# Performance work log

Hardware: AMD Instinct MI355X
Metric: run time of the kernel (lower is better)

The kernel has to match this reference:

```python
import jax, jax.numpy as jnp
import numpy as np

P_TOKENS = 200  # num_prompt_tokens
N_HEADS = 4


def setup_inputs() -> dict:
    key = jax.random.key(0)
    ks = jax.random.split(key, 6)
    B, N, C = 64, 1224, 1024
    D = 256  # bottleneck / down_size
    s = 0.02
    return {
        "x": jax.random.normal(ks[0], (B, N, C), dtype=jnp.float32),
        "down_W": jax.random.normal(ks[1], (D, C), dtype=jnp.float32) * s,
        "down_b": jnp.zeros((D,), jnp.float32),
        "up_W": jax.random.normal(ks[2], (C, D), dtype=jnp.float32) * s,
        "up_b": jnp.zeros((C,), jnp.float32),
        "in_proj_W": jax.random.normal(ks[3], (3 * D, D), dtype=jnp.float32) * s,
        "in_proj_b": jnp.zeros((3 * D,), jnp.float32),
        "out_proj_W": jax.random.normal(ks[4], (D, D), dtype=jnp.float32) * s,
        "out_proj_b": jnp.zeros((D,), jnp.float32),
        "gate": jnp.float32(1.0),
    }


def _forward(x, down_W, down_b, up_W, up_b, in_proj_W, in_proj_b,
             out_proj_W, out_proj_b, gate):
    B, N, C = x.shape
    E = down_W.shape[0]
    hd = E // N_HEADS
    # down projection + exact GELU (torch nn.GELU default)
    down = jax.nn.gelu(x @ down_W.T + down_b, approximate=False)  # [B,N,E]
    prompt = down[:, :P_TOKENS, :]   # [B,P,E]
    tok = down[:, P_TOKENS:, :]      # [B,T,E]
    # --- nn.MultiheadAttention(prompt, prompt, prompt) ---
    qkv = prompt @ in_proj_W.T + in_proj_b            # [B,P,3E]
    q, k, v = jnp.split(qkv, 3, axis=-1)
    def heads(t):
        return t.reshape(B, P_TOKENS, N_HEADS, hd)
    q, k, v = heads(q), heads(k), heads(v)
    attn = jnp.einsum('bqhd,bkhd->bhqk', q, k) / jnp.sqrt(jnp.float32(hd))
    attn = jax.nn.softmax(attn, axis=-1)
    sa = jnp.einsum('bhqk,bkhd->bqhd', attn, v).reshape(B, P_TOKENS, E)
    sa = sa @ out_proj_W.T + out_proj_b               # [B,P,E]
    # --- manual cross attention prompt -> tokens ---
    scale = jnp.float32(E) ** -0.5
    cross = jax.nn.softmax(jnp.einsum('bpe,bte->bpt', sa, tok) * scale, axis=-1)
    prompt_out = jnp.einsum('bpt,bte->bpe', cross, tok)  # [B,P,E]
    combined = jnp.concatenate([prompt_out, tok], axis=1)  # [B,N,E]
    up = combined @ up_W.T + up_b                          # [B,N,C]
    return gate * up


def reference(x, down_W, down_b, up_W, up_b, in_proj_W, in_proj_b,
              out_proj_W, out_proj_b, gate):
    return _forward(x, down_W, down_b, up_W, up_b, in_proj_W, in_proj_b,
                    out_proj_W, out_proj_b, gate)
```

## Files before the change

### kernel.cpp

```cpp
#include <hip/hip_runtime.h>
#include <math.h>

#define BB 64
#define NN 1224
#define CC 1024
#define DD 256
#define PP 200
#define TT 1024
#define HH 4
#define HDD 64

typedef __attribute__((ext_vector_type(8))) short bf16x8;
typedef __attribute__((ext_vector_type(4))) float f32x4;
typedef unsigned short u16;
typedef unsigned long long u64;

__device__ __forceinline__ u16 f2bf(float f) {
  union { float f; unsigned int u; } v; v.f = f;
  unsigned int r = v.u + 0x7FFF + ((v.u >> 16) & 1);
  return (u16)(r >> 16);
}
__device__ __forceinline__ float bf2f(u16 h) {
  union { unsigned int u; float f; } v; v.u = ((unsigned int)h) << 16;
  return v.f;
}
__device__ __forceinline__ unsigned int pk2(float a, float b) {
  return (unsigned int)f2bf(a) | ((unsigned int)f2bf(b) << 16);
}
__device__ __forceinline__ void gload16(const void* g, void* l) {
  __builtin_amdgcn_global_load_lds(
      (const __attribute__((address_space(1))) void*)g,
      (__attribute__((address_space(3))) void*)l, 16, 0, 0);
}

static const size_t SZ_DOWN = (size_t)BB * NN * DD * 2;
static const size_t SZ_TOKT = (size_t)BB * DD * TT * 2;
static const size_t SZ_Q    = (size_t)BB * HH * PP * HDD * 2;
static const size_t SZ_SCORES = (size_t)BB * PP * TT * 2;

static const size_t B_DOWN   = 0;
static const size_t B_TOKT   = B_DOWN + SZ_DOWN;
static const size_t B_POOL   = B_TOKT + SZ_TOKT;
static const size_t B_QB     = B_POOL;
static const size_t B_KB     = B_QB + SZ_Q;
static const size_t B_VB     = B_KB + SZ_Q;
static const size_t B_SA     = B_VB + SZ_Q;
static const size_t B_SA2    = B_SA + SZ_Q;
static const size_t B_PBF    = B_POOL;
static const size_t B_POUTBF = B_SA2;
static const size_t B_SCORES = B_SA2 + SZ_Q;
static const size_t B_W      = B_SCORES + SZ_SCORES * 2;
static const size_t B_WD     = B_W;
static const size_t B_WU     = B_WD + 524288;
static const size_t B_WIP    = B_WU + 524288;
static const size_t B_WOP    = B_WIP + 393216;

#define GEMM_VARS \
  const int tid = threadIdx.x; \
  const int lane = tid & 63, wave = tid >> 6; \
  const int wm = wave >> 2, wn = wave & 3; \
  f32x4 acc[4][4] = {};

#define MFMA_STEP(Ab, Bb) \
  _Pragma("unroll") \
  for (int kk = 0; kk < 64; kk += 32) { \
    bf16x8 af[4], bfr[4]; \
    _Pragma("unroll") \
    for (int mi = 0; mi < 4; ++mi) { \
      const int R = wm * 64 + mi * 16 + (lane & 15); \
      const int byt = (R * 128 + (kk + (lane >> 4) * 8) * 2) ^ ((R & 7) << 4); \
      af[mi] = *(const bf16x8*)((const char*)Ab + byt); \
    } \
    _Pragma("unroll") \
    for (int ni = 0; ni < 4; ++ni) { \
      const int R = wn * 64 + ni * 16 + (lane & 15); \
      const int byt = (R * 128 + (kk + (lane >> 4) * 8) * 2) ^ ((R & 7) << 4); \
      bfr[ni] = *(const bf16x8*)((const char*)Bb + byt); \
    } \
    _Pragma("unroll") \
    for (int mi = 0; mi < 4; ++mi) \
      _Pragma("unroll") \
      for (int ni = 0; ni < 4; ++ni) \
        acc[mi][ni] = __builtin_amdgcn_mfma_f32_16x16x32_bf16(af[mi], bfr[ni], acc[mi][ni], 0, 0, 0); \
  }

#define GLOAD_A2(Ab, SRC) \
  _Pragma("unroll") \
  for (int ii = 0; ii < 2; ++ii) { \
    const int slot = wave * 2 + ii; \
    const int L = slot * 1024 + lane * 16; \
    const int r = L >> 7; \
    const int ce = ((L & 127) ^ ((r & 7) << 4)) >> 1; \
    gload16((SRC), (char*)Ab + slot * 1024); \
  }

#define GLOAD_B4(Bb, SRC) \
  _Pragma("unroll") \
  for (int ii = 0; ii < 4; ++ii) { \
    const int slot = wave * 4 + ii; \
    const int L = slot * 1024 + lane * 16; \
    const int r = L >> 7; \
    const int ce = ((L & 127) ^ ((r & 7) << 4)) >> 1; \
    gload16((SRC), (char*)Bb + slot * 1024); \
  }

#define MFMA_STEP64(Ab, Bb) \
  _Pragma("unroll") \
  for (int kk = 0; kk < 64; kk += 32) { \
    bf16x8 af[4], bfr[2]; \
    _Pragma("unroll") \
    for (int mi = 0; mi < 4; ++mi) { \
      const int R = mi * 16 + (lane & 15); \
      const int byt = (R * 128 + (kk + (lane >> 4) * 8) * 2) ^ ((R & 7) << 4); \
      af[mi] = *(const bf16x8*)((const char*)Ab + byt); \
    } \
    _Pragma("unroll") \
    for (int ni = 0; ni < 2; ++ni) { \
      const int R = wave * 32 + ni * 16 + (lane & 15); \
      const int byt = (R * 128 + (kk + (lane >> 4) * 8) * 2) ^ ((R & 7) << 4); \
      bfr[ni] = *(const bf16x8*)((const char*)Bb + byt); \
    } \
    _Pragma("unroll") \
    for (int mi = 0; mi < 4; ++mi) \
      _Pragma("unroll") \
      for (int ni = 0; ni < 2; ++ni) \
        acc[mi][ni] = __builtin_amdgcn_mfma_f32_16x16x32_bf16(af[mi], bfr[ni], acc[mi][ni], 0, 0, 0); \
  }

#define GLOAD_A1(Ab, SRC) \
  { \
    const int L = wave * 1024 + lane * 16; \
    const int r = L >> 7; \
    const int ce = ((L & 127) ^ ((r & 7) << 4)) >> 1; \
    gload16((SRC), (char*)Ab + wave * 1024); \
  }

__global__ __launch_bounds__(256) void k_castw(const float* __restrict__ dW,
                                               const float* __restrict__ uW,
                                               const float* __restrict__ iW,
                                               const float* __restrict__ oW,
                                               u16* __restrict__ dWb, u16* __restrict__ uWb,
                                               u16* __restrict__ iWb, u16* __restrict__ oWb)
{
  const int id = blockIdx.x * 256 + threadIdx.x;
  const float* s; u16* d; int off;
  if (id < 65536)       { s = dW; d = dWb; off = id; }
  else if (id < 131072) { s = uW; d = uWb; off = id - 65536; }
  else if (id < 180224) { s = iW; d = iWb; off = id - 131072; }
  else                  { s = oW; d = oWb; off = id - 180224; }
  const float4 v = ((const float4*)s)[off];
  uint2 p; p.x = pk2(v.x, v.y); p.y = pk2(v.z, v.w);
  *(uint2*)&d[(size_t)off * 4] = p;
}

__global__ __launch_bounds__(512, 6) void k_down(const float* __restrict__ x,
                                                 const u16* __restrict__ Wd,
                                                 const float* __restrict__ bias,
                                                 u16* __restrict__ out)
{
  __shared__ u16 Ab[64 * 64];
  __shared__ u16 Bb[256 * 64];
  const int tid = threadIdx.x;
  const int lane = tid & 63, wave = tid >> 6;
  f32x4 acc[4][2] = {};
  const int m0 = blockIdx.x * 64;
  const int ar0 = tid >> 4;
  const int c4 = (tid & 15) * 4;

  float4 areg[2];
#pragma unroll
  for (int i = 0; i < 2; ++i)
    areg[i] = *(const float4*)&x[(size_t)(m0 + ar0 + 32 * i) * CC + c4];

  for (int k0 = 0; k0 < CC; k0 += 64) {
    GLOAD_B4(Bb, &Wd[(size_t)r * CC + k0 + ce])
#pragma unroll
    for (int i = 0; i < 2; ++i) {
      const int r = ar0 + 32 * i;
      uint2 p; p.x = pk2(areg[i].x, areg[i].y); p.y = pk2(areg[i].z, areg[i].w);
      const int byt = (r * 128 + c4 * 2) ^ ((r & 7) << 4);
      *(uint2*)((char*)Ab + byt) = p;
    }
    __syncthreads();
    if (k0 + 64 < CC) {
#pragma unroll
      for (int i = 0; i < 2; ++i)
        areg[i] = *(const float4*)&x[(size_t)(m0 + ar0 + 32 * i) * CC + k0 + 64 + c4];
    }
    MFMA_STEP64(Ab, Bb)
    __syncthreads();
  }
#pragma unroll
  for (int mi = 0; mi < 4; ++mi) {
#pragma unroll
    for (int ni = 0; ni < 2; ++ni) {
      const int col = wave * 32 + ni * 16 + (lane & 15);
      const float bv = bias[col];
#pragma unroll
      for (int r = 0; r < 4; ++r) {
        const int row = m0 + mi * 16 + (lane >> 4) * 4 + r;
        float v = acc[mi][ni][r] + bv;
        v = 0.5f * v * (1.f + erff(v * 0.7071067811865475f));
        out[(size_t)row * DD + col] = f2bf(v);
      }
    }
  }
}

__global__ __launch_bounds__(256) void k_tokT(const u16* __restrict__ down,
                                              u16* __restrict__ tokT)
{
  __shared__ u16 Ls[64][68];
  const int b = blockIdx.z;
  const int t0 = blockIdx.x * 64, e0 = blockIdx.y * 64;
  const int tid = threadIdx.x;
#pragma unroll
  for (int it = 0; it < 4; ++it) {
    const int idx = tid + 256 * it;
    const int r = idx >> 4, c4 = (idx & 15) * 4;
    const u64 v = *(const u64*)&down[((size_t)(b * NN + PP + t0 + r)) * DD + e0 + c4];
    *(u64*)&Ls[r][c4] = v;
  }
  __syncthreads();
#pragma unroll
  for (int it = 0; it < 4; ++it) {
    const int idx = tid + 256 * it;
    const int re = idx >> 4, c4 = (idx & 15) * 4;
    u64 pk = (u64)Ls[c4 + 0][re] | ((u64)Ls[c4 + 1][re] << 16) |
             ((u64)Ls[c4 + 2][re] << 32) | ((u64)Ls[c4 + 3][re] << 48);
    *(u64*)&tokT[((size_t)(b * DD + e0 + re)) * TT + t0 + c4] = pk;
  }
}

__global__ __launch_bounds__(512) void k_qkv(const u16* __restrict__ down,
                                             const u16* __restrict__ Wip,
                                             const float* __restrict__ bias,
                                             u16* __restrict__ qb,
                                             u16* __restrict__ kb,
                                             u16* __restrict__ vb)
{
  __shared__ u16 Ab[128 * 64];
  __shared__ u16 Bb[256 * 64];
  GEMM_VARS
  const int m0 = blockIdx.x * 128;
  const int nt = blockIdx.y;

  for (int k0 = 0; k0 < DD; k0 += 64) {
    GLOAD_A2(Ab, ({ const int m = m0 + r; const int b = m / PP; const int p = m - b * PP;
                    &down[((size_t)(b * NN + p)) * DD + k0 + ce]; }))
    GLOAD_B4(Bb, &Wip[(size_t)(nt * 256 + r) * DD + k0 + ce])
    __syncthreads();
    MFMA_STEP(Ab, Bb)
    __syncthreads();
  }
  u16* dst = (nt == 0) ? qb : ((nt == 1) ? kb : vb);
#pragma unroll
  for (int mi = 0; mi < 4; ++mi) {
#pragma unroll
    for (int ni = 0; ni < 4; ++ni) {
      const int n = wn * 64 + ni * 16 + (lane & 15);
      const float bv = bias[nt * 256 + n];
      const int h = n >> 6, dd = n & 63;
#pragma unroll
      for (int r = 0; r < 4; ++r) {
        const int m = m0 + wm * 64 + mi * 16 + (lane >> 4) * 4 + r;
        const int b = m / PP, p = m - b * PP;
        dst[(((size_t)(b * HH + h)) * PP + p) * HDD + dd] = f2bf(acc[mi][ni][r] + bv);
      }
    }
  }
}

__global__ __launch_bounds__(256) void k_attn(const u16* __restrict__ qb,
                                              const u16* __restrict__ kb,
                                              const u16* __restrict__ vb,
                                              u16* __restrict__ sa)
{
  __shared__ u16 Ks[208 * 64];
  __shared__ u16 Vt[64 * 232];
  __shared__ u16 Pb[4 * 16 * 232];
  const int tid = threadIdx.x, lane = tid & 63, wave = tid >> 6;
  const int bh = blockIdx.x;
  const size_t kvbase = (size_t)bh * (PP * HDD);

  for (int it = 0; it < 13; ++it) {
    const int idx = tid + 256 * it;
    if (idx < 3200) {
      const int e = idx * 4;
      const int j = e >> 6, d = e & 63;
      const u64 kv = *(const u64*)&kb[kvbase + e];
      const int byt = (j * 128 + d * 2) ^ ((j & 7) << 4);
      *(u64*)((char*)Ks + byt) = kv;
      const u64 vv = *(const u64*)&vb[kvbase + e];
      const u16* vp = (const u16*)&vv;
#pragma unroll
      for (int w = 0; w < 4; ++w) Vt[(d + w) * 232 + j] = vp[w];
    }
  }
  if (tid < 128) {
    const int rr = 200 + (tid >> 4), c = (tid & 15) * 4;
    const int byt = (rr * 128 + c * 2) ^ ((rr & 7) << 4);
    *(u64*)((char*)Ks + byt) = 0ULL;
  }
#pragma unroll
  for (int w = 0; w < 2; ++w) {
    const int idx = tid + 256 * w;
    const int d = idx >> 3, cg = idx & 7;
    *(u64*)&Vt[d * 232 + 200 + cg * 4] = 0ULL;
  }
  {
    u16* pw = Pb + wave * (16 * 232);
#pragma unroll
    for (int w = 0; w < 2; ++w) {
      const int idx = lane + 64 * w;
      if (idx < 96) {
        const int row = idx / 6, cg = idx - row * 6;
        *(u64*)&pw[row * 232 + 208 + cg * 4] = 0ULL;
      }
    }
  }
  __syncthreads();

  const int b_ = bh >> 2, h = bh & 3;
  const u16* qbase = qb + kvbase;
  u16* pw = Pb + wave * (16 * 232);

  for (int f = wave; f < 13; f += 4) {
    int qrow = f * 16 + (lane & 15); if (qrow > 199) qrow = 199;
    bf16x8 qa[2];
#pragma unroll
    for (int kk = 0; kk < 2; ++kk)
      qa[kk] = *(const bf16x8*)&qbase[(size_t)qrow * 64 + kk * 32 + (lane >> 4) * 8];

    f32x4 s[13];
#pragma unroll
    for (int nf = 0; nf < 13; ++nf) {
      const int R = nf * 16 + (lane & 15);
      f32x4 a = {};
#pragma unroll
      for (int kk = 0; kk < 2; ++kk) {
        const int byt = (R * 128 + (kk * 32 + (lane >> 4) * 8) * 2) ^ ((R & 7) << 4);
        const bf16x8 kf = *(const bf16x8*)((const char*)Ks + byt);
        a = __builtin_amdgcn_mfma_f32_16x16x32_bf16(qa[kk], kf, a, 0, 0, 0);
      }
      s[nf] = a;
    }
    float mx[4] = {-1e30f, -1e30f, -1e30f, -1e30f};
#pragma unroll
    for (int nf = 0; nf < 13; ++nf) {
      const int col = nf * 16 + (lane & 15);
#pragma unroll
      for (int r = 0; r < 4; ++r) {
        float v = (col < PP) ? s[nf][r] * 0.125f : -INFINITY;
        s[nf][r] = v;
        mx[r] = fmaxf(mx[r], v);
      }
    }
#pragma unroll
    for (int off = 1; off < 16; off <<= 1)
#pragma unroll
      for (int r = 0; r < 4; ++r) mx[r] = fmaxf(mx[r], __shfl_xor(mx[r], off));
    float sum[4] = {0.f, 0.f, 0.f, 0.f};
#pragma unroll
    for (int nf = 0; nf < 13; ++nf)
#pragma unroll
      for (int r = 0; r < 4; ++r) {
        const float e = expf(s[nf][r] - mx[r]);
        s[nf][r] = e;
        sum[r] += e;
      }
#pragma unroll
    for (int off = 1; off < 16; off <<= 1)
#pragma unroll
      for (int r = 0; r < 4; ++r) sum[r] += __shfl_xor(sum[r], off);
    float inv[4];
#pragma unroll
    for (int r = 0; r < 4; ++r) inv[r] = 1.f / sum[r];
#pragma unroll
    for (int nf = 0; nf < 13; ++nf) {
      const int col = nf * 16 + (lane & 15);
#pragma unroll
      for (int r = 0; r < 4; ++r) {
        const int row = (lane >> 4) * 4 + r;
        pw[row * 232 + col] = f2bf(s[nf][r] * inv[r]);
      }
    }
    f32x4 o[4] = {};
#pragma unroll
    for (int kk = 0; kk < 7; ++kk) {
      const bf16x8 pa = *(const bf16x8*)((const char*)pw +
                         ((lane & 15) * 232 + kk * 32 + (lane >> 4) * 8) * 2);
#pragma unroll
      for (int nf4 = 0; nf4 < 4; ++nf4) {
        const bf16x8 vv = *(const bf16x8*)((const char*)Vt +
                           (((lane & 15) + 16 * nf4) * 232 + kk * 32 + (lane >> 4) * 8) * 2);
        o[nf4] = __builtin_amdgcn_mfma_f32_16x16x32_bf16(pa, vv, o[nf4], 0, 0, 0);
      }
    }
#pragma unroll
    for (int nf4 = 0; nf4 < 4; ++nf4) {
      const int d = (lane & 15) + 16 * nf4;
#pragma unroll
      for (int r = 0; r < 4; ++r) {
        const int p = f * 16 + (lane >> 4) * 4 + r;
        if (p < PP)
          sa[((size_t)(b_ * PP + p)) * DD + h * HDD + d] = f2bf(o[nf4][r]);
      }
    }
  }
}

__global__ __launch_bounds__(512) void k_oproj(const u16* __restrict__ A,
                                               const u16* __restrict__ Wop,
                                               const float* __restrict__ bias,
                                               u16* __restrict__ out)
{
  __shared__ u16 Ab[128 * 64];
  __shared__ u16 Bb[256 * 64];
  GEMM_VARS
  const int m0 = blockIdx.x * 128;

  for (int k0 = 0; k0 < DD; k0 += 64) {
    GLOAD_A2(Ab, &A[(size_t)(m0 + r) * DD + k0 + ce])
    GLOAD_B4(Bb, &Wop[(size_t)r * DD + k0 + ce])
    __syncthreads();
    MFMA_STEP(Ab, Bb)
    __syncthreads();
  }
#pragma unroll
  for (int mi = 0; mi < 4; ++mi) {
#pragma unroll
    for (int ni = 0; ni < 4; ++ni) {
      const int col = wn * 64 + ni * 16 + (lane & 15);
      const float bv = bias[col];
#pragma unroll
      for (int r = 0; r < 4; ++r) {
        const int row = m0 + wm * 64 + mi * 16 + (lane >> 4) * 4 + r;
        out[(size_t)row * DD + col] = f2bf(acc[mi][ni][r] + bv);
      }
    }
  }
}

__global__ __launch_bounds__(512) void k_scores(const u16* __restrict__ sa2,
                                                const u16* __restrict__ down,
                                                u16* __restrict__ scores)
{
  __shared__ u16 Ab[128 * 64];
  __shared__ u16 Bb[256 * 64];
  GEMM_VARS
  const int b = blockIdx.x, mh = blockIdx.y, nt = blockIdx.z;

  for (int k0 = 0; k0 < DD; k0 += 64) {
    GLOAD_A2(Ab, ({ int p = mh * 128 + r; p = (p < PP) ? p : (PP - 1);
                    &sa2[((size_t)(b * PP + p)) * DD + k0 + ce]; }))
    GLOAD_B4(Bb, &down[((size_t)(b * NN + PP + nt * 256 + r)) * DD + k0 + ce])
    __syncthreads();
    MFMA_STEP(Ab, Bb)
    __syncthreads();
  }
#pragma unroll
  for (int mi = 0; mi < 4; ++mi) {
#pragma unroll
    for (int ni = 0; ni < 4; ++ni) {
      const int t = nt * 256 + wn * 64 + ni * 16 + (lane & 15);
#pragma unroll
      for (int r = 0; r < 4; ++r) {
        const int p = mh * 128 + wm * 64 + mi * 16 + (lane >> 4) * 4 + r;
        if (p < PP)
          scores[((size_t)(b * PP + p)) * TT + t] = f2bf(acc[mi][ni][r] * 0.0625f);
      }
    }
  }
}

__global__ __launch_bounds__(256) void k_softmax(const u16* __restrict__ s,
                                                 u16* __restrict__ pbf)
{
  const int row = blockIdx.x;
  const int t = threadIdx.x;
  const int lane = t & 63, w = t >> 6;
  __shared__ float red[4];
  const u64 raw = *(const u64*)&s[(size_t)row * TT + t * 4];
  float v[4];
#pragma unroll
  for (int i = 0; i < 4; ++i) v[i] = bf2f((u16)(raw >> (16 * i)));
  float mx = fmaxf(fmaxf(v[0], v[1]), fmaxf(v[2], v[3]));
#pragma unroll
  for (int off = 32; off; off >>= 1) mx = fmaxf(mx, __shfl_xor(mx, off));
  if (lane == 0) red[w] = mx;
  __syncthreads();
  mx = fmaxf(fmaxf(red[0], red[1]), fmaxf(red[2], red[3]));
  __syncthreads();
  float sum = 0.f;
#pragma unroll
  for (int i = 0; i < 4; ++i) { v[i] = expf(v[i] - mx); sum += v[i]; }
#pragma unroll
  for (int off = 32; off; off >>= 1) sum += __shfl_xor(sum, off);
  if (lane == 0) red[w] = sum;
  __syncthreads();
  sum = red[0] + red[1] + red[2] + red[3];
  const float inv = 1.f / sum;
  u64 pk = (u64)f2bf(v[0] * inv) | ((u64)f2bf(v[1] * inv) << 16) |
           ((u64)f2bf(v[2] * inv) << 32) | ((u64)f2bf(v[3] * inv) << 48);
  *(u64*)&pbf[(size_t)row * TT + t * 4] = pk;
}

__global__ __launch_bounds__(512) void k_pout(const u16* __restrict__ pbf,
                                              const u16* __restrict__ tokT,
                                              u16* __restrict__ out)
{
  __shared__ u16 Ab[128 * 64];
  __shared__ u16 Bb[256 * 64];
  GEMM_VARS
  const int b = blockIdx.x, mh = blockIdx.y;

  for (int k0 = 0; k0 < TT; k0 += 64) {
    GLOAD_A2(Ab, ({ int p = mh * 128 + r; p = (p < PP) ? p : (PP - 1);
                    &pbf[((size_t)(b * PP + p)) * TT + k0 + ce]; }))
    GLOAD_B4(Bb, &tokT[((size_t)(b * DD + r)) * TT + k0 + ce])
    __syncthreads();
    MFMA_STEP(Ab, Bb)
    __syncthreads();
  }
#pragma unroll
  for (int mi = 0; mi < 4; ++mi) {
#pragma unroll
    for (int ni = 0; ni < 4; ++ni) {
      const int e = wn * 64 + ni * 16 + (lane & 15);
#pragma unroll
      for (int r = 0; r < 4; ++r) {
        const int p = mh * 128 + wm * 64 + mi * 16 + (lane >> 4) * 4 + r;
        if (p < PP)
          out[((size_t)(b * PP + p)) * DD + e] = f2bf(acc[mi][ni][r]);
      }
    }
  }
}

__global__ __launch_bounds__(512, 6) void k_up(const u16* __restrict__ poutbf,
                                               const u16* __restrict__ down,
                                               const u16* __restrict__ Wu,
                                               const float* __restrict__ bias,
                                               const float* __restrict__ gate,
                                               float* __restrict__ out)
{
  __shared__ u16 Ab[64 * 64];
  __shared__ u16 Bb[256 * 64];
  const int tid = threadIdx.x;
  const int lane = tid & 63, wave = tid >> 6;
  f32x4 acc[4][2] = {};
  const int m0 = blockIdx.x * 64;
  const int n0 = blockIdx.y * 256;

  for (int k0 = 0; k0 < DD; k0 += 64) {
    GLOAD_A1(Ab, ({ const int m = m0 + r; const int b = m / NN; const int rr = m - b * NN;
                    const u16* base = (rr < PP) ? &poutbf[((size_t)(b * PP + rr)) * DD]
                                                : &down[((size_t)(b * NN + rr)) * DD];
                    base + k0 + ce; }))
    GLOAD_B4(Bb, &Wu[(size_t)(n0 + r) * DD + k0 + ce])
    __syncthreads();
    MFMA_STEP64(Ab, Bb)
    __syncthreads();
  }
  const float g = gate[0];
#pragma unroll
  for (int mi = 0; mi < 4; ++mi) {
#pragma unroll
    for (int ni = 0; ni < 2; ++ni) {
      const int col = n0 + wave * 32 + ni * 16 + (lane & 15);
      const float bv = bias[col];
#pragma unroll
      for (int r = 0; r < 4; ++r) {
        const int row = m0 + mi * 16 + (lane >> 4) * 4 + r;
        out[(size_t)row * CC + col] = (acc[mi][ni][r] + bv) * g;
      }
    }
  }
}

extern "C" void kernel_launch(void* const* d_in, const int* in_sizes, int n_in,
                              void* d_out, int out_size, void* d_ws, size_t ws_size,
                              hipStream_t stream) {
  const float* x          = (const float*)d_in[0];
  const float* down_W     = (const float*)d_in[1];
  const float* down_b     = (const float*)d_in[2];
  const float* up_W       = (const float*)d_in[3];
  const float* up_b       = (const float*)d_in[4];
  const float* in_proj_W  = (const float*)d_in[5];
  const float* in_proj_b  = (const float*)d_in[6];
  const float* out_proj_W = (const float*)d_in[7];
  const float* out_proj_b = (const float*)d_in[8];
  const float* gate       = (const float*)d_in[9];
  float* out = (float*)d_out;

  char* wsb = (char*)d_ws;
  u16* down_bf = (u16*)(wsb + B_DOWN);
  u16* tokT    = (u16*)(wsb + B_TOKT);
  u16* qb      = (u16*)(wsb + B_QB);
  u16* kb      = (u16*)(wsb + B_KB);
  u16* vb      = (u16*)(wsb + B_VB);
  u16* sa_bf   = (u16*)(wsb + B_SA);
  u16* sa2_bf  = (u16*)(wsb + B_SA2);
  u16* pbf     = (u16*)(wsb + B_PBF);
  u16* poutbf  = (u16*)(wsb + B_POUTBF);
  u16* scores  = (u16*)(wsb + B_SCORES);
  u16* Wd  = (u16*)(wsb + B_WD);
  u16* Wu  = (u16*)(wsb + B_WU);
  u16* Wip = (u16*)(wsb + B_WIP);
  u16* Wop = (u16*)(wsb + B_WOP);

  k_castw<<<dim3(768), 256, 0, stream>>>(down_W, up_W, in_proj_W, out_proj_W, Wd, Wu, Wip, Wop);
  k_down<<<dim3((BB * NN) / 64), 512, 0, stream>>>(x, Wd, down_b, down_bf);
  k_tokT<<<dim3(16, 4, BB), 256, 0, stream>>>(down_bf, tokT);
  k_qkv<<<dim3(100, 3), 512, 0, stream>>>(down_bf, Wip, in_proj_b, qb, kb, vb);
  k_attn<<<dim3(BB * HH), 256, 0, stream>>>(qb, kb, vb, sa_bf);
  k_oproj<<<dim3(100), 512, 0, stream>>>(sa_bf, Wop, out_proj_b, sa2_bf);
  k_scores<<<dim3(BB, 2, 4), 512, 0, stream>>>(sa2_bf, down_bf, scores);
  k_softmax<<<dim3(BB * PP), 256, 0, stream>>>(scores, pbf);
  k_pout<<<dim3(BB, 2), 512, 0, stream>>>(pbf, tokT, poutbf);
  k_up<<<dim3((BB * NN) / 64, CC / 256), 512, 0, stream>>>(poutbf, down_bf, Wu, up_b, gate, out);
}
```

Baseline: 371.9 us.

## Fuse cross-attention scores, softmax and PV into one flash-style kernel

Replaces the three-kernel cross-attention path (scores GEMM, row softmax, P·tok GEMM) with a single kernel per batch and 16-prompt tile. Scores stay in registers, softmax is reduced through LDS across waves, and the bf16 probabilities are staged in swizzled LDS before the PV MFMA. This removes the global round trips of the scores and probability matrices and two launches. In exchange it reads K/V fragments straight from global memory without LDS tiling and gives only 832 blocks of 4 waves, which may limit operand reuse and occupancy.

```diff
diff --git a/kernel.cpp b/kernel.cpp
--- a/kernel.cpp
+++ b/kernel.cpp
@@ -46,10 +46,8 @@
 static const size_t B_VB     = B_KB + SZ_Q;
 static const size_t B_SA     = B_VB + SZ_Q;
 static const size_t B_SA2    = B_SA + SZ_Q;
-static const size_t B_PBF    = B_POOL;
-static const size_t B_POUTBF = B_SA2;
-static const size_t B_SCORES = B_SA2 + SZ_Q;
-static const size_t B_W      = B_SCORES + SZ_SCORES * 2;
+static const size_t B_POUT   = B_SA2 + SZ_Q;
+static const size_t B_W      = B_POUT + SZ_SCORES * 2;
 static const size_t B_WD     = B_W;
 static const size_t B_WU     = B_WD + 524288;
 static const size_t B_WIP    = B_WU + 524288;
@@ -442,98 +440,118 @@
   }
 }
 
-__global__ __launch_bounds__(512) void k_scores(const u16* __restrict__ sa2,
-                                                const u16* __restrict__ down,
-                                                u16* __restrict__ scores)
-{
-  __shared__ u16 Ab[128 * 64];
-  __shared__ u16 Bb[256 * 64];
-  GEMM_VARS
-  const int b = blockIdx.x, mh = blockIdx.y, nt = blockIdx.z;
-
-  for (int k0 = 0; k0 < DD; k0 += 64) {
-    GLOAD_A2(Ab, ({ int p = mh * 128 + r; p = (p < PP) ? p : (PP - 1);
-                    &sa2[((size_t)(b * PP + p)) * DD + k0 + ce]; }))
-    GLOAD_B4(Bb, &down[((size_t)(b * NN + PP + nt * 256 + r)) * DD + k0 + ce])
-    __syncthreads();
-    MFMA_STEP(Ab, Bb)
-    __syncthreads();
-  }
-#pragma unroll
-  for (int mi = 0; mi < 4; ++mi) {
-#pragma unroll
-    for (int ni = 0; ni < 4; ++ni) {
-      const int t = nt * 256 + wn * 64 + ni * 16 + (lane & 15);
-#pragma unroll
-      for (int r = 0; r < 4; ++r) {
-        const int p = mh * 128 + wm * 64 + mi * 16 + (lane >> 4) * 4 + r;
-        if (p < PP)
-          scores[((size_t)(b * PP + p)) * TT + t] = f2bf(acc[mi][ni][r] * 0.0625f);
-      }
-    }
-  }
-}
-
-__global__ __launch_bounds__(256) void k_softmax(const u16* __restrict__ s,
-                                                 u16* __restrict__ pbf)
-{
-  const int row = blockIdx.x;
-  const int t = threadIdx.x;
-  const int lane = t & 63, w = t >> 6;
-  __shared__ float red[4];
-  const u64 raw = *(const u64*)&s[(size_t)row * TT + t * 4];
-  float v[4];
-#pragma unroll
-  for (int i = 0; i < 4; ++i) v[i] = bf2f((u16)(raw >> (16 * i)));
-  float mx = fmaxf(fmaxf(v[0], v[1]), fmaxf(v[2], v[3]));
-#pragma unroll
-  for (int off = 32; off; off >>= 1) mx = fmaxf(mx, __shfl_xor(mx, off));
-  if (lane == 0) red[w] = mx;
+__global__ __launch_bounds__(256) void k_cross(const u16* __restrict__ sa2,
+                                               const u16* __restrict__ down,
+                                               const u16* __restrict__ tokT,
+                                               u16* __restrict__ pout)
+{
+  __shared__ u16 Pl[16 * 1024];
+  __shared__ float Mred[4][16];
+  __shared__ float Lred[4][16];
+  const int tid = threadIdx.x, lane = tid & 63, wave = tid >> 6;
+  const int b = blockIdx.x, pf = blockIdx.y;
+
+  int qrow = pf * 16 + (lane & 15); if (qrow > PP - 1) qrow = PP - 1;
+  const u16* qp = &sa2[((size_t)(b * PP + qrow)) * DD];
+  bf16x8 q[8];
+#pragma unroll
+  for (int kk = 0; kk < 8; ++kk)
+    q[kk] = *(const bf16x8*)&qp[kk * 32 + (lane >> 4) * 8];
+
+  const int t0 = wave * 256;
+  const u16* tokb = &down[((size_t)(b * NN + PP)) * DD];
+  f32x4 s[16];
+#pragma unroll
+  for (int nf = 0; nf < 16; ++nf) {
+    const int trow = t0 + nf * 16 + (lane & 15);
+    const u16* kp = &tokb[(size_t)trow * DD];
+    f32x4 a = {};
+#pragma unroll
+    for (int kk = 0; kk < 8; ++kk) {
+      const bf16x8 kf = *(const bf16x8*)&kp[kk * 32 + (lane >> 4) * 8];
+      a = __builtin_amdgcn_mfma_f32_16x16x32_bf16(q[kk], kf, a, 0, 0, 0);
+    }
+    s[nf] = a;
+  }
+  float mx[4] = {-1e30f, -1e30f, -1e30f, -1e30f};
+#pragma unroll
+  for (int nf = 0; nf < 16; ++nf)
+#pragma unroll
+    for (int r = 0; r < 4; ++r) {
+      const float v = s[nf][r] * 0.0625f;
+      s[nf][r] = v;
+      mx[r] = fmaxf(mx[r], v);
+    }
+#pragma unroll
+  for (int off = 1; off < 16; off <<= 1)
+#pragma unroll
+    for (int r = 0; r < 4; ++r) mx[r] = fmaxf(mx[r], __shfl_xor(mx[r], off));
+  if ((lane & 15) == 0) {
+#pragma unroll
+    for (int r = 0; r < 4; ++r) Mred[wave][(lane >> 4) * 4 + r] = mx[r];
+  }
   __syncthreads();
-  mx = fmaxf(fmaxf(red[0], red[1]), fmaxf(red[2], red[3]));
+  float M[4];
+#pragma unroll
+  for (int r = 0; r < 4; ++r) {
+    const int row = (lane >> 4) * 4 + r;
+    M[r] = fmaxf(fmaxf(Mred[0][row], Mred[1][row]), fmaxf(Mred[2][row], Mred[3][row]));
+  }
+  float l[4] = {0.f, 0.f, 0.f, 0.f};
+#pragma unroll
+  for (int nf = 0; nf < 16; ++nf)
+#pragma unroll
+    for (int r = 0; r < 4; ++r) {
+      const float e = __expf(s[nf][r] - M[r]);
+      s[nf][r] = e;
+      l[r] += e;
+    }
+#pragma unroll
+  for (int off = 1; off < 16; off <<= 1)
+#pragma unroll
+    for (int r = 0; r < 4; ++r) l[r] += __shfl_xor(l[r], off);
+  if ((lane & 15) == 0) {
+#pragma unroll
+    for (int r = 0; r < 4; ++r) Lred[wave][(lane >> 4) * 4 + r] = l[r];
+  }
+#pragma unroll
+  for (int nf = 0; nf < 16; ++nf) {
+    const int tcol = t0 + nf * 16 + (lane & 15);
+#pragma unroll
+    for (int r = 0; r < 4; ++r) {
+      const int prow = (lane >> 4) * 4 + r;
+      *(u16*)((char*)Pl + ((prow * 2048 + tcol * 2) ^ ((prow & 7) << 4))) = f2bf(s[nf][r]);
+    }
+  }
   __syncthreads();
-  float sum = 0.f;
-#pragma unroll
-  for (int i = 0; i < 4; ++i) { v[i] = expf(v[i] - mx); sum += v[i]; }
-#pragma unroll
-  for (int off = 32; off; off >>= 1) sum += __shfl_xor(sum, off);
-  if (lane == 0) red[w] = sum;
-  __syncthreads();
-  sum = red[0] + red[1] + red[2] + red[3];
-  const float inv = 1.f / sum;
-  u64 pk = (u64)f2bf(v[0] * inv) | ((u64)f2bf(v[1] * inv) << 16) |
-           ((u64)f2bf(v[2] * inv) << 32) | ((u64)f2bf(v[3] * inv) << 48);
-  *(u64*)&pbf[(size_t)row * TT + t * 4] = pk;
-}
-
-__global__ __launch_bounds__(512) void k_pout(const u16* __restrict__ pbf,
-                                              const u16* __restrict__ tokT,
-                                              u16* __restrict__ out)
-{
-  __shared__ u16 Ab[128 * 64];
-  __shared__ u16 Bb[256 * 64];
-  GEMM_VARS
-  const int b = blockIdx.x, mh = blockIdx.y;
-
-  for (int k0 = 0; k0 < TT; k0 += 64) {
-    GLOAD_A2(Ab, ({ int p = mh * 128 + r; p = (p < PP) ? p : (PP - 1);
-                    &pbf[((size_t)(b * PP + p)) * TT + k0 + ce]; }))
-    GLOAD_B4(Bb, &tokT[((size_t)(b * DD + r)) * TT + k0 + ce])
-    __syncthreads();
-    MFMA_STEP(Ab, Bb)
-    __syncthreads();
-  }
-#pragma unroll
-  for (int mi = 0; mi < 4; ++mi) {
-#pragma unroll
-    for (int ni = 0; ni < 4; ++ni) {
-      const int e = wn * 64 + ni * 16 + (lane & 15);
-#pragma unroll
-      for (int r = 0; r < 4; ++r) {
-        const int p = mh * 128 + wm * 64 + mi * 16 + (lane >> 4) * 4 + r;
-        if (p < PP)
-          out[((size_t)(b * PP + p)) * DD + e] = f2bf(acc[mi][ni][r]);
-      }
+  float Ltot[4];
+#pragma unroll
+  for (int r = 0; r < 4; ++r) {
+    const int row = (lane >> 4) * 4 + r;
+    Ltot[r] = Lred[0][row] + Lred[1][row] + Lred[2][row] + Lred[3][row];
+  }
+  const u16* vbp = &tokT[((size_t)(b * DD + wave * 64)) * TT];
+  f32x4 o[4] = {};
+#pragma unroll
+  for (int kc = 0; kc < 32; ++kc) {
+    const int prow = lane & 15;
+    const int byt = ((prow * 2048 + (kc * 32 + (lane >> 4) * 8) * 2)) ^ ((prow & 7) << 4);
+    const bf16x8 pa = *(const bf16x8*)((const char*)Pl + byt);
+#pragma unroll
+    for (int nf = 0; nf < 4; ++nf) {
+      const int erow = nf * 16 + (lane & 15);
+      const bf16x8 vf = *(const bf16x8*)&vbp[(size_t)erow * TT + kc * 32 + (lane >> 4) * 8];
+      o[nf] = __builtin_amdgcn_mfma_f32_16x16x32_bf16(pa, vf, o[nf], 0, 0, 0);
+    }
+  }
+#pragma unroll
+  for (int nf = 0; nf < 4; ++nf) {
+    const int e = wave * 64 + nf * 16 + (lane & 15);
+#pragma unroll
+    for (int r = 0; r < 4; ++r) {
+      const int p = pf * 16 + (lane >> 4) * 4 + r;
+      if (p < PP)
+        pout[((size_t)(b * PP + p)) * DD + e] = f2bf(o[nf][r] * (1.f / Ltot[r]));
     }
   }
 }
@@ -602,9 +620,7 @@
   u16* vb      = (u16*)(wsb + B_VB);
   u16* sa_bf   = (u16*)(wsb + B_SA);
   u16* sa2_bf  = (u16*)(wsb + B_SA2);
-  u16* pbf     = (u16*)(wsb + B_PBF);
-  u16* poutbf  = (u16*)(wsb + B_POUTBF);
-  u16* scores  = (u16*)(wsb + B_SCORES);
+  u16* poutbf  = (u16*)(wsb + B_POUT);
   u16* Wd  = (u16*)(wsb + B_WD);
   u16* Wu  = (u16*)(wsb + B_WU);
   u16* Wip = (u16*)(wsb + B_WIP);
@@ -616,8 +632,6 @@
   k_qkv<<<dim3(100, 3), 512, 0, stream>>>(down_bf, Wip, in_proj_b, qb, kb, vb);
   k_attn<<<dim3(BB * HH), 256, 0, stream>>>(qb, kb, vb, sa_bf);
   k_oproj<<<dim3(100), 512, 0, stream>>>(sa_bf, Wop, out_proj_b, sa2_bf);
-  k_scores<<<dim3(BB, 2, 4), 512, 0, stream>>>(sa2_bf, down_bf, scores);
-  k_softmax<<<dim3(BB * PP), 256, 0, stream>>>(scores, pbf);
-  k_pout<<<dim3(BB, 2), 512, 0, stream>>>(pbf, tokT, poutbf);
+  k_cross<<<dim3(BB, 13), 256, 0, stream>>>(sa2_bf, down_bf, tokT, poutbf);
   k_up<<<dim3((BB * NN) / 64, CC / 256), 512, 0, stream>>>(poutbf, down_bf, Wu, up_b, gate, out);
 }
```

Result: slower. 435.2 us (+17.0%).

## Double-buffer LDS in down and up projection GEMMs with manual waitcnt

Applied to the files above, without the earlier changes.

Converts k_down and k_up from single-buffered LDS tiles with two __syncthreads per k-step into double-buffered pipelines. The next tile's global-to-LDS loads are issued before the MFMA step on the current buffer, and explicit s_waitcnt vmcnt counts plus sched_barriers control the ordering. This aims to hide global load latency behind matrix compute. In exchange LDS use doubles (80KB per block) and the occupancy hint of 6 is dropped, which lowers blocks per CU. The hand-set vmcnt values must match the exact number of loads the macros issue, or the result can be wrong.

```diff
diff --git a/kernel.cpp b/kernel.cpp
--- a/kernel.cpp
+++ b/kernel.cpp
@@ -153,13 +153,13 @@
   *(uint2*)&d[(size_t)off * 4] = p;
 }
 
-__global__ __launch_bounds__(512, 6) void k_down(const float* __restrict__ x,
-                                                 const u16* __restrict__ Wd,
-                                                 const float* __restrict__ bias,
-                                                 u16* __restrict__ out)
-{
-  __shared__ u16 Ab[64 * 64];
-  __shared__ u16 Bb[256 * 64];
+__global__ __launch_bounds__(512) void k_down(const float* __restrict__ x,
+                                              const u16* __restrict__ Wd,
+                                              const float* __restrict__ bias,
+                                              u16* __restrict__ out)
+{
+  __shared__ u16 Ab[2][64 * 64];
+  __shared__ u16 Bb[2][256 * 64];
   const int tid = threadIdx.x;
   const int lane = tid & 63, wave = tid >> 6;
   f32x4 acc[4][2] = {};
@@ -171,24 +171,51 @@
 #pragma unroll
   for (int i = 0; i < 2; ++i)
     areg[i] = *(const float4*)&x[(size_t)(m0 + ar0 + 32 * i) * CC + c4];
-
-  for (int k0 = 0; k0 < CC; k0 += 64) {
-    GLOAD_B4(Bb, &Wd[(size_t)r * CC + k0 + ce])
-#pragma unroll
-    for (int i = 0; i < 2; ++i) {
-      const int r = ar0 + 32 * i;
-      uint2 p; p.x = pk2(areg[i].x, areg[i].y); p.y = pk2(areg[i].z, areg[i].w);
-      const int byt = (r * 128 + c4 * 2) ^ ((r & 7) << 4);
-      *(uint2*)((char*)Ab + byt) = p;
-    }
-    __syncthreads();
-    if (k0 + 64 < CC) {
+#pragma unroll
+  for (int i = 0; i < 2; ++i) {
+    const int r = ar0 + 32 * i;
+    uint2 p; p.x = pk2(areg[i].x, areg[i].y); p.y = pk2(areg[i].z, areg[i].w);
+    *(uint2*)((char*)Ab[0] + ((r * 128 + c4 * 2) ^ ((r & 7) << 4))) = p;
+  }
+  GLOAD_B4(Bb[0], &Wd[(size_t)r * CC + 0 + ce])
+#pragma unroll
+  for (int i = 0; i < 2; ++i)
+    areg[i] = *(const float4*)&x[(size_t)(m0 + ar0 + 32 * i) * CC + 64 + c4];
+
+  for (int it = 0; it < 16; ++it) {
+    const int cur = it & 1;
+    if (it < 14) {
+#pragma unroll
+      for (int i = 0; i < 2; ++i) {
+        const int r = ar0 + 32 * i;
+        uint2 p; p.x = pk2(areg[i].x, areg[i].y); p.y = pk2(areg[i].z, areg[i].w);
+        *(uint2*)((char*)Ab[cur ^ 1] + ((r * 128 + c4 * 2) ^ ((r & 7) << 4))) = p;
+      }
+      const int kx = (it + 2) * 64;
 #pragma unroll
       for (int i = 0; i < 2; ++i)
-        areg[i] = *(const float4*)&x[(size_t)(m0 + ar0 + 32 * i) * CC + k0 + 64 + c4];
-    }
-    MFMA_STEP64(Ab, Bb)
-    __syncthreads();
+        areg[i] = *(const float4*)&x[(size_t)(m0 + ar0 + 32 * i) * CC + kx + c4];
+      const int kb = (it + 1) * 64;
+      GLOAD_B4(Bb[cur ^ 1], &Wd[(size_t)r * CC + kb + ce])
+      asm volatile("s_waitcnt vmcnt(6) lgkmcnt(0)" ::: "memory");
+    } else if (it == 14) {
+#pragma unroll
+      for (int i = 0; i < 2; ++i) {
+        const int r = ar0 + 32 * i;
+        uint2 p; p.x = pk2(areg[i].x, areg[i].y); p.y = pk2(areg[i].z, areg[i].w);
+        *(uint2*)((char*)Ab[cur ^ 1] + ((r * 128 + c4 * 2) ^ ((r & 7) << 4))) = p;
+      }
+      GLOAD_B4(Bb[cur ^ 1], &Wd[(size_t)r * CC + 960 + ce])
+      asm volatile("s_waitcnt vmcnt(4) lgkmcnt(0)" ::: "memory");
+    } else {
+      asm volatile("s_waitcnt vmcnt(0) lgkmcnt(0)" ::: "memory");
+    }
+    __builtin_amdgcn_s_barrier();
+    __builtin_amdgcn_sched_barrier(0);
+    MFMA_STEP64(Ab[cur], Bb[cur])
+    asm volatile("s_waitcnt lgkmcnt(0)" ::: "memory");
+    __builtin_amdgcn_s_barrier();
+    __builtin_amdgcn_sched_barrier(0);
   }
 #pragma unroll
   for (int mi = 0; mi < 4; ++mi) {
@@ -538,30 +565,46 @@
   }
 }
 
-__global__ __launch_bounds__(512, 6) void k_up(const u16* __restrict__ poutbf,
-                                               const u16* __restrict__ down,
-                                               const u16* __restrict__ Wu,
-                                               const float* __restrict__ bias,
-                                               const float* __restrict__ gate,
-                                               float* __restrict__ out)
-{
-  __shared__ u16 Ab[64 * 64];
-  __shared__ u16 Bb[256 * 64];
+__global__ __launch_bounds__(512) void k_up(const u16* __restrict__ poutbf,
+                                            const u16* __restrict__ down,
+                                            const u16* __restrict__ Wu,
+                                            const float* __restrict__ bias,
+                                            const float* __restrict__ gate,
+                                            float* __restrict__ out)
+{
+  __shared__ u16 Ab[2][64 * 64];
+  __shared__ u16 Bb[2][256 * 64];
   const int tid = threadIdx.x;
   const int lane = tid & 63, wave = tid >> 6;
   f32x4 acc[4][2] = {};
   const int m0 = blockIdx.x * 64;
   const int n0 = blockIdx.y * 256;
 
-  for (int k0 = 0; k0 < DD; k0 += 64) {
-    GLOAD_A1(Ab, ({ const int m = m0 + r; const int b = m / NN; const int rr = m - b * NN;
-                    const u16* base = (rr < PP) ? &poutbf[((size_t)(b * PP + rr)) * DD]
-                                                : &down[((size_t)(b * NN + rr)) * DD];
-                    base + k0 + ce; }))
-    GLOAD_B4(Bb, &Wu[(size_t)(n0 + r) * DD + k0 + ce])
-    __syncthreads();
-    MFMA_STEP64(Ab, Bb)
-    __syncthreads();
+  GLOAD_A1(Ab[0], ({ const int m = m0 + r; const int b = m / NN; const int rr = m - b * NN;
+                     const u16* base = (rr < PP) ? &poutbf[((size_t)(b * PP + rr)) * DD]
+                                                 : &down[((size_t)(b * NN + rr)) * DD];
+                     base + 0 + ce; }))
+  GLOAD_B4(Bb[0], &Wu[(size_t)(n0 + r) * DD + 0 + ce])
+
+  for (int it = 0; it < 4; ++it) {
+    const int cur = it & 1;
+    if (it < 3) {
+      const int k0 = (it + 1) * 64;
+      GLOAD_A1(Ab[cur ^ 1], ({ const int m = m0 + r; const int b = m / NN; const int rr = m - b * NN;
+                               const u16* base = (rr < PP) ? &poutbf[((size_t)(b * PP + rr)) * DD]
+                                                           : &down[((size_t)(b * NN + rr)) * DD];
+                               base + k0 + ce; }))
+      GLOAD_B4(Bb[cur ^ 1], &Wu[(size_t)(n0 + r) * DD + k0 + ce])
+      asm volatile("s_waitcnt vmcnt(5)" ::: "memory");
+    } else {
+      asm volatile("s_waitcnt vmcnt(0)" ::: "memory");
+    }
+    __builtin_amdgcn_s_barrier();
+    __builtin_amdgcn_sched_barrier(0);
+    MFMA_STEP64(Ab[cur], Bb[cur])
+    asm volatile("s_waitcnt lgkmcnt(0)" ::: "memory");
+    __builtin_amdgcn_s_barrier();
+    __builtin_amdgcn_sched_barrier(0);
   }
   const float g = gate[0];
 #pragma unroll
```

Result: faster. 356.3 us (-4.2%).
